# Performance work log

Hardware: AMD Instinct MI355X
Metric: run time of the kernel (lower is better)

## Reference

```python
import jax, jax.numpy as jnp
import numpy as np

DIM, K_NN, RADIUS, HIDDEN = 128, 4, 2.5, 64
B, T, N = 32, 64, 25


def setup_inputs() -> dict:
    key = jax.random.key(0)
    ks = jax.random.split(key, 12)
    s = 0.02
    return {
        "emb": jax.random.normal(ks[0], (B, T, N, DIM), jnp.float32),
        "bboxes": jax.random.uniform(ks[1], (B, T, N, 4), jnp.float32),
        "person_mask": jax.random.uniform(ks[2], (B, T, N)) < 0.9,
        "edge_w1": jax.random.normal(ks[3], (2 * DIM + 3, HIDDEN), jnp.float32) * s,
        "edge_b1": jnp.zeros((HIDDEN,), jnp.float32),
        "edge_w2": jax.random.normal(ks[4], (HIDDEN, DIM), jnp.float32) * s,
        "edge_b2": jnp.zeros((DIM,), jnp.float32),
        "node_w1": jax.random.normal(ks[5], (2 * DIM, HIDDEN), jnp.float32) * s,
        "node_b1": jnp.zeros((HIDDEN,), jnp.float32),
        "node_w2": jax.random.normal(ks[6], (HIDDEN, DIM), jnp.float32) * s,
        "node_b2": jnp.zeros((DIM,), jnp.float32),
        "ln_g": jnp.ones((DIM,), jnp.float32),
        "ln_b": jnp.zeros((DIM,), jnp.float32),
    }


def _forward(emb, bboxes, person_mask, edge_w1, edge_b1, edge_w2, edge_b2,
             node_w1, node_b1, node_w2, node_b2, ln_g, ln_b):
    b, t, n, d = emb.shape
    BT = b * t
    x = emb.reshape(BT, n, d)
    boxes = bboxes.reshape(BT, n, 4)
    mask = person_mask.reshape(BT, n)

    cx, cy = boxes[..., 0], boxes[..., 1]
    h = jnp.maximum(boxes[..., 3], 1e-6)
    dx = cx[:, :, None] - cx[:, None, :]            # [BT,N,N]
    dy = cy[:, :, None] - cy[:, None, :]
    dist = jnp.sqrt(dx * dx + dy * dy + 1e-6)
    scale = h[:, :, None]
    dx_n, dy_n, dist_n = dx / scale, dy / scale, dist / scale

    eye = jnp.eye(n, dtype=bool)[None]
    pair_valid = (mask[:, :, None] & mask[:, None, :]) & ~eye
    dist_for_knn = jnp.where(pair_valid, dist_n, 1e6)

    K = min(K_NN, max(n - 1, 1))
    neg_d, knn_idx = jax.lax.top_k(-dist_for_knn, K)  # smallest-K -> [BT,N,K]
    knn_dist = -neg_d

    nbr_valid = jnp.take_along_axis(pair_valid, knn_idx, axis=2)
    nbr_valid = nbr_valid & (knn_dist < RADIUS)

    # gather neighbor features: [BT,N,K,D]
    bt_idx = jnp.arange(BT)[:, None, None]
    x_j = x[bt_idx, knn_idx]
    x_i = jnp.broadcast_to(x[:, :, None, :], (BT, n, K, d))
    edge_all = jnp.stack([dx_n, dy_n, dist_n], axis=-1)  # [BT,N,N,3]
    e_ij = jnp.take_along_axis(edge_all, knn_idx[..., None], axis=2)  # [BT,N,K,3]

    msg_in = jnp.concatenate([x_i, x_j, e_ij], axis=-1)  # [BT,N,K,2D+3]
    msg = jax.nn.relu(msg_in @ edge_w1 + edge_b1) @ edge_w2 + edge_b2
    nbr_f = nbr_valid.astype(msg.dtype)
    msg = msg * nbr_f[..., None]
    denom = jnp.maximum(nbr_f.sum(axis=2, keepdims=True), 1.0)
    agg = msg.sum(axis=2) / denom                    # [BT,N,D]

    upd_in = jnp.concatenate([x, agg], axis=-1)
    delta = jax.nn.relu(upd_in @ node_w1 + node_b1) @ node_w2 + node_b2
    has_nbr = jnp.any(nbr_valid, axis=2, keepdims=True)
    delta = delta * has_nbr.astype(delta.dtype)

    y = x + delta
    mu = y.mean(axis=-1, keepdims=True)
    var = y.var(axis=-1, keepdims=True)
    y = (y - mu) * jax.lax.rsqrt(var + 1e-5) * ln_g + ln_b
    out = y * mask[..., None].astype(y.dtype)
    return out.reshape(b, t, n, d)


def reference(emb, bboxes, person_mask, edge_w1, edge_b1, edge_w2, edge_b2,
              node_w1, node_b1, node_w2, node_b2, ln_g, ln_b):
    return _forward(emb, bboxes, person_mask, edge_w1, edge_b1, edge_w2, edge_b2,
                    node_w1, node_b1, node_w2, node_b2, ln_g, ln_b)
```

## Files before the change

### kernel.cpp

```cpp
#include <hip/hip_runtime.h>

#define NN   25
#define DD   128
#define HH   64
#define KK   4
#define RADF 2.5f

#define XBP  136
#define HSP  72

#define O_W1T  0
#define O_W2NT 16896
#define O_N1LO 20992
#define O_N2T  29184
#define O_B2N  37376

typedef __attribute__((ext_vector_type(8))) short  short8;
typedef __attribute__((ext_vector_type(4))) float  f32x4;

__device__ __forceinline__ ushort f2bf(float x) {
    uint u = __float_as_uint(x);
    u += 0x7fffu + ((u >> 16) & 1u);
    return (ushort)(u >> 16);
}
__device__ __forceinline__ float bf2f(ushort u) {
    return __uint_as_float((uint)u << 16);
}
__device__ __forceinline__ uint pack2(float a, float b) {
    return (uint)f2bf(a) | ((uint)f2bf(b) << 16);
}
__device__ __forceinline__ short8 ldw(const ushort* p) {
    return *reinterpret_cast<const short8*>(p);
}
#define MFMA16(a, b, c) __builtin_amdgcn_mfma_f32_16x16x32_bf16((a), (b), (c), 0, 0, 0)

__global__ void prep_kernel(const float* __restrict__ ew1, const float* __restrict__ ew2,
                            const float* __restrict__ eb2, const float* __restrict__ nw1,
                            const float* __restrict__ nw2, ushort* __restrict__ w) {
    int tid = blockIdx.x * blockDim.x + threadIdx.x;
    int stride = gridDim.x * blockDim.x;
    for (int e = tid; e < 259 * 64; e += stride) {
        int k = e >> 6, c = e & 63;
        w[O_W1T + c * 264 + k] = f2bf(ew1[e]);
    }
    for (int e = tid; e < 64 * 128; e += stride) {
        int c = e >> 7, k = e & 127;
        w[O_N1LO + e] = f2bf(nw1[(size_t)k * 64 + c]);
    }
    for (int e = tid; e < 128 * 64; e += stride) {
        int d = e >> 6, k = e & 63;
        w[O_N2T + e] = f2bf(nw2[(size_t)k * 128 + d]);
    }
    for (int e = tid; e < 64 * 64; e += stride) {
        int c = e >> 6, k = e & 63;
        float acc = 0.f;
        for (int d = 0; d < DD; ++d)
            acc += ew2[(size_t)k * DD + d] * nw1[(size_t)(DD + d) * HH + c];
        w[O_W2NT + e] = f2bf(acc);
    }
    for (int c = tid; c < HH; c += stride) {
        float acc = 0.f;
        for (int d = 0; d < DD; ++d)
            acc += eb2[d] * nw1[(size_t)(DD + d) * HH + c];
        reinterpret_cast<float*>(w + O_B2N)[c] = acc;
    }
}

__global__ __launch_bounds__(128, 4) void ig12_kernel(
    const float* __restrict__ emb,
    const float* __restrict__ bboxes,
    const int*   __restrict__ pmask,
    const float* __restrict__ ew1f,
    const float* __restrict__ eb1,
    const float* __restrict__ nb1,
    const float* __restrict__ nb2,
    const float* __restrict__ lng,
    const float* __restrict__ lnb,
    const ushort* __restrict__ W,
    float* __restrict__ out)
{
    const int bt  = blockIdx.x;
    const int t   = threadIdx.x;
    const int wv  = t >> 6;
    const int ln  = t & 63;
    const int g   = ln >> 4;
    const int r16 = ln & 15;
    const int cb  = 2 * wv;
    const int cb4 = 4 * wv;

    __shared__ ushort s_xb[NN * XBP];
    __shared__ ushort s_hxi[NN * HSP];
    __shared__ ushort s_hs[NN * HSP];
    __shared__ ushort s_nxi[NN * HSP];
    __shared__ __align__(16) char s_misc[1600];
    __shared__ short  s_idxs[NN][KK];
    __shared__ float  s_meta[NN][4];

    float (*s_ev)[KK][4] = reinterpret_cast<float(*)[KK][4]>(s_misc);
    float (*s_red)[2][2] = reinterpret_cast<float(*)[2][2]>(s_misc);
    ushort* s_g1v = s_hxi;

    if (wv == 0) {
        const float4* src4 = reinterpret_cast<const float4*>(emb + (size_t)bt * (NN * DD));
        for (int u = ln; u < NN * 16; u += 64) {
            int row = u >> 4, q = u & 15;
            float4 f0 = src4[row * 32 + q * 2];
            float4 f1 = src4[row * 32 + q * 2 + 1];
            uint4 p;
            p.x = pack2(f0.x, f0.y); p.y = pack2(f0.z, f0.w);
            p.z = pack2(f1.x, f1.y); p.w = pack2(f1.z, f1.w);
            *reinterpret_cast<uint4*>(&s_xb[row * XBP + q * 8]) = p;
        }
    } else {
        const int n = (ln < NN) ? ln : NN - 1;
        const float4 b4 = *reinterpret_cast<const float4*>(bboxes + ((size_t)bt * NN + n) * 4);
        const float cxn = b4.x, cyn = b4.y;
        const float hvn = fmaxf(b4.w, 1e-6f);
        const int   mn  = pmask[(size_t)bt * NN + n];
        const float inv = 1.0f / hvn;
        float best[KK] = {1e30f, 1e30f, 1e30f, 1e30f};
        int   bidx[KK] = {0, 0, 0, 0};
        for (int j = 0; j < NN; ++j) {
            float cxj = __shfl(cxn, j);
            float cyj = __shfl(cyn, j);
            int   mj  = __shfl(mn, j);
            float dx = cxn - cxj, dy = cyn - cyj;
            float dn = sqrtf(fmaf(dx, dx, fmaf(dy, dy, 1e-6f))) * inv;
            bool  pv = (mn != 0) && (mj != 0) && (j != n);
            float cv = pv ? dn : 1e6f;
            int   ci = j;
#pragma unroll
            for (int kk = 0; kk < KK; ++kk) {
                if (cv < best[kk]) {
                    float tv = best[kk]; best[kk] = cv; cv = tv;
                    int   ti = bidx[kk]; bidx[kk] = ci; ci = ti;
                }
            }
        }
        float cnt = 0.f;
        float e0v[KK], e1v[KK], e2v[KK], vvv[KK];
#pragma unroll
        for (int k = 0; k < KK; ++k) {
            int bj = bidx[k];
            float cxb = __shfl(cxn, bj);
            float cyb = __shfl(cyn, bj);
            float val = (best[k] < RADF) ? 1.f : 0.f;
            cnt += val;
            float dx = cxn - cxb, dy = cyn - cyb;
            e0v[k] = dx * inv;
            e1v[k] = dy * inv;
            e2v[k] = sqrtf(fmaf(dx, dx, fmaf(dy, dy, 1e-6f))) * inv;
            vvv[k] = val;
        }
        if (ln < NN) {
#pragma unroll
            for (int k = 0; k < KK; ++k) {
                s_ev[n][k][0] = e0v[k];
                s_ev[n][k][1] = e1v[k];
                s_ev[n][k][2] = e2v[k];
                s_ev[n][k][3] = vvv[k];
                s_idxs[n][k]  = (short)bidx[k];
            }
            s_meta[n][0] = cnt;
            s_meta[n][1] = 1.0f / fmaxf(cnt, 1.0f);
            s_meta[n][2] = (cnt > 0.f) ? 1.f : 0.f;
            s_meta[n][3] = mn ? 1.f : 0.f;
        }
    }
    __syncthreads();

    {
        int na1 = 16 + r16; if (na1 > 24) na1 = 24;
        const ushort* A0 = s_xb + r16 * XBP + g * 8;
        const ushort* A1 = s_xb + na1 * XBP + g * 8;
        f32x4 ce[2][2] = {};
        f32x4 cn[2][2] = {};
#pragma unroll
        for (int kt = 0; kt < 4; ++kt) {
            short8 a0 = ldw(A0 + kt * 32);
            short8 a1 = ldw(A1 + kt * 32);
#pragma unroll
            for (int ntl = 0; ntl < 2; ++ntl) {
                short8 be = ldw(W + O_W1T  + (size_t)(16 * (cb + ntl) + r16) * 264 + kt * 32 + g * 8);
                short8 bn = ldw(W + O_N1LO + (size_t)(16 * (cb + ntl) + r16) * 128 + kt * 32 + g * 8);
                ce[0][ntl] = MFMA16(a0, be, ce[0][ntl]);
                ce[1][ntl] = MFMA16(a1, be, ce[1][ntl]);
                cn[0][ntl] = MFMA16(a0, bn, cn[0][ntl]);
                cn[1][ntl] = MFMA16(a1, bn, cn[1][ntl]);
            }
        }
#pragma unroll
        for (int mt = 0; mt < 2; ++mt)
#pragma unroll
            for (int q = 0; q < 4; ++q) {
                int nr = 16 * mt + 4 * g + q;
                if (nr < 25) {
#pragma unroll
                    for (int ntl = 0; ntl < 2; ++ntl) {
                        int col = 16 * (cb + ntl) + r16;
                        s_hxi[nr * HSP + col] = f2bf(ce[mt][ntl][q]);
                        s_nxi[nr * HSP + col] = f2bf(cn[mt][ntl][q]);
                    }
                }
            }
    }

    {
        int jn[7];
#pragma unroll
        for (int T = 0; T < 7; ++T) {
            int r = 16 * T + r16; if (r > 99) r = 99;
            jn[T] = s_idxs[r >> 2][r & 3];
        }
        f32x4 c[7][2] = {};
#pragma unroll
        for (int kt = 0; kt < 4; ++kt) {
            short8 b0 = ldw(W + O_W1T + (size_t)(16 * (cb + 0) + r16) * 264 + 128 + kt * 32 + g * 8);
            short8 b1 = ldw(W + O_W1T + (size_t)(16 * (cb + 1) + r16) * 264 + 128 + kt * 32 + g * 8);
#pragma unroll
            for (int T = 0; T < 7; ++T) {
                short8 a = ldw(s_xb + jn[T] * XBP + kt * 32 + g * 8);
                c[T][0] = MFMA16(a, b0, c[T][0]);
                c[T][1] = MFMA16(a, b1, c[T][1]);
            }
        }
        float we0[2], we1[2], we2[2], bb1[2];
#pragma unroll
        for (int ntl = 0; ntl < 2; ++ntl) {
            int col = 16 * (cb + ntl) + r16;
            we0[ntl] = ew1f[256 * 64 + col];
            we1[ntl] = ew1f[257 * 64 + col];
            we2[ntl] = ew1f[258 * 64 + col];
            bb1[ntl] = eb1[col];
        }
#pragma unroll
        for (int T = 0; T < 7; ++T) {
            const int n = 4 * T + g;
            if (n < 25) {
                float v0 = s_ev[n][0][3], v1 = s_ev[n][1][3];
                float v2 = s_ev[n][2][3], v3 = s_ev[n][3][3];
                float e0q[4], e1q[4], e2q[4];
#pragma unroll
                for (int q = 0; q < 4; ++q) {
                    e0q[q] = s_ev[n][q][0]; e1q[q] = s_ev[n][q][1]; e2q[q] = s_ev[n][q][2];
                }
#pragma unroll
                for (int ntl = 0; ntl < 2; ++ntl) {
                    int col = 16 * (cb + ntl) + r16;
                    float base = bb1[ntl] + bf2f(s_hxi[n * HSP + col]);
                    float p0 = c[T][ntl][0] + base + e0q[0] * we0[ntl] + e1q[0] * we1[ntl] + e2q[0] * we2[ntl];
                    float p1 = c[T][ntl][1] + base + e0q[1] * we0[ntl] + e1q[1] * we1[ntl] + e2q[1] * we2[ntl];
                    float p2 = c[T][ntl][2] + base + e0q[2] * we0[ntl] + e1q[2] * we1[ntl] + e2q[2] * we2[ntl];
                    float p3 = c[T][ntl][3] + base + e0q[3] * we0[ntl] + e1q[3] * we1[ntl] + e2q[3] * we2[ntl];
                    float hs = fmaf(v0, fmaxf(p0, 0.f),
                               fmaf(v1, fmaxf(p1, 0.f),
                               fmaf(v2, fmaxf(p2, 0.f),
                                    v3 * fmaxf(p3, 0.f))));
                    s_hs[n * HSP + col] = f2bf(hs);
                }
            }
        }
    }
    __syncthreads();

    {
        int na1 = 16 + r16; if (na1 > 24) na1 = 24;
        const ushort* A0 = s_hs + r16 * HSP + g * 8;
        const ushort* A1 = s_hs + na1 * HSP + g * 8;
        f32x4 c[2][2] = {};
#pragma unroll
        for (int kt = 0; kt < 2; ++kt) {
            short8 a0 = ldw(A0 + kt * 32);
            short8 a1 = ldw(A1 + kt * 32);
#pragma unroll
            for (int ntl = 0; ntl < 2; ++ntl) {
                short8 b = ldw(W + O_W2NT + (size_t)(16 * (cb + ntl) + r16) * 64 + kt * 32 + g * 8);
                c[0][ntl] = MFMA16(a0, b, c[0][ntl]);
                c[1][ntl] = MFMA16(a1, b, c[1][ntl]);
            }
        }
        const float* b2Np = reinterpret_cast<const float*>(W + O_B2N);
#pragma unroll
        for (int ntl = 0; ntl < 2; ++ntl) {
            int col = 16 * (cb + ntl) + r16;
            float b2n = b2Np[col];
            float b1c = nb1[col];
#pragma unroll
            for (int mt = 0; mt < 2; ++mt)
#pragma unroll
                for (int q = 0; q < 4; ++q) {
                    int nr = 16 * mt + 4 * g + q;
                    if (nr < 25) {
                        float v = bf2f(s_nxi[nr * HSP + col]) + b1c
                                + s_meta[nr][1] * fmaf(s_meta[nr][0], b2n, c[mt][ntl][q]);
                        s_g1v[nr * HSP + col] = f2bf(fmaxf(v, 0.f));
                    }
                }
        }
    }
    __syncthreads();

    {
        int na1 = 16 + r16; if (na1 > 24) na1 = 24;
        const ushort* A0 = s_g1v + r16 * HSP + g * 8;
        const ushort* A1 = s_g1v + na1 * HSP + g * 8;
        f32x4 c[2][4] = {};
#pragma unroll
        for (int kt = 0; kt < 2; ++kt) {
            short8 a0 = ldw(A0 + kt * 32);
            short8 a1 = ldw(A1 + kt * 32);
#pragma unroll
            for (int ntl = 0; ntl < 4; ++ntl) {
                short8 b = ldw(W + O_N2T + (size_t)(16 * (cb4 + ntl) + r16) * 64 + kt * 32 + g * 8);
                c[0][ntl] = MFMA16(a0, b, c[0][ntl]);
                c[1][ntl] = MFMA16(a1, b, c[1][ntl]);
            }
        }
        float nb2c[4], glc[4], blc[4];
#pragma unroll
        for (int ntl = 0; ntl < 4; ++ntl) {
            int col = 16 * (cb4 + ntl) + r16;
            nb2c[ntl] = nb2[col];
            glc[ntl]  = lng[col];
            blc[ntl]  = lnb[col];
        }
        float y[2][4][4];
#pragma unroll
        for (int mt = 0; mt < 2; ++mt) {
#pragma unroll
            for (int q = 0; q < 4; ++q) {
                int nr = 16 * mt + 4 * g + q;
                int nc = nr < 25 ? nr : 24;
                float has = s_meta[nc][2];
                float a = 0.f, b = 0.f;
#pragma unroll
                for (int ntl = 0; ntl < 4; ++ntl) {
                    int col = 16 * (cb4 + ntl) + r16;
                    float yv = fmaf(has, c[mt][ntl][q] + nb2c[ntl], bf2f(s_xb[nc * XBP + col]));
                    y[mt][ntl][q] = yv;
                    a += yv;
                    b = fmaf(yv, yv, b);
                }
#pragma unroll
                for (int o = 1; o < 16; o <<= 1) {
                    a += __shfl_xor(a, o);
                    b += __shfl_xor(b, o);
                }
                if (r16 == 0 && nr < 25) {
                    s_red[nr][wv][0] = a;
                    s_red[nr][wv][1] = b;
                }
            }
        }
        __syncthreads();
#pragma unroll
        for (int mt = 0; mt < 2; ++mt) {
#pragma unroll
            for (int q = 0; q < 4; ++q) {
                int nr = 16 * mt + 4 * g + q;
                int nc = nr < 25 ? nr : 24;
                float S   = s_red[nc][0][0] + s_red[nc][1][0];
                float S2  = s_red[nc][0][1] + s_red[nc][1][1];
                float mu  = S * (1.0f / 128.0f);
                float var = S2 * (1.0f / 128.0f) - mu * mu;
                float rs  = rsqrtf(var + 1e-5f);
                float mk  = s_meta[nc][3];
                if (nr < 25) {
                    float* op = out + (size_t)bt * (NN * DD) + nr * DD;
#pragma unroll
                    for (int ntl = 0; ntl < 4; ++ntl) {
                        int col = 16 * (cb4 + ntl) + r16;
                        op[col] = fmaf((y[mt][ntl][q] - mu) * rs, glc[ntl], blc[ntl]) * mk;
                    }
                }
            }
        }
    }
}

extern "C" void kernel_launch(void* const* d_in, const int* in_sizes, int n_in,
                              void* d_out, int out_size, void* d_ws, size_t ws_size,
                              hipStream_t stream) {
    const float* emb    = (const float*)d_in[0];
    const float* bboxes = (const float*)d_in[1];
    const int*   pmask  = (const int*)  d_in[2];
    const float* ew1    = (const float*)d_in[3];
    const float* eb1    = (const float*)d_in[4];
    const float* ew2    = (const float*)d_in[5];
    const float* eb2    = (const float*)d_in[6];
    const float* nw1    = (const float*)d_in[7];
    const float* nb1    = (const float*)d_in[8];
    const float* nw2    = (const float*)d_in[9];
    const float* nb2    = (const float*)d_in[10];
    const float* lng    = (const float*)d_in[11];
    const float* lnb    = (const float*)d_in[12];
    float* out = (float*)d_out;
    ushort* W  = (ushort*)d_ws;

    prep_kernel<<<64, 256, 0, stream>>>(ew1, ew2, eb2, nw1, nw2, W);

    const int BT = in_sizes[2] / NN;
    ig12_kernel<<<BT, 128, 0, stream>>>(
        emb, bboxes, pmask, ew1, eb1, nb1, nb2, lng, lnb, W, out);
}
```

Before: 42.73 us.

## Keep node pre-activation in registers, prefetch weights across barriers, use LDS-only barriers

The node-MLP x-part accumulator stays in registers instead of round-tripping through a shared buffer, which removes that LDS array and its stores and loads. Global weight and bias loads for the next two GEMM stages are issued before each barrier so their latency overlaps the barrier wait. __syncthreads is replaced by an explicit lgkmcnt(0) wait plus s_barrier, so the barrier does not wait on outstanding global loads. The cost is higher register pressure from live accumulators and prefetched fragments, which could reduce occupancy or cause spills.

```diff
diff --git a/kernel.cpp b/kernel.cpp
--- a/kernel.cpp
+++ b/kernel.cpp
@@ -33,6 +33,11 @@
     return *reinterpret_cast<const short8*>(p);
 }
 #define MFMA16(a, b, c) __builtin_amdgcn_mfma_f32_16x16x32_bf16((a), (b), (c), 0, 0, 0)
+
+#define BAR_LGKM() do {                                      \
+    asm volatile("s_waitcnt lgkmcnt(0)" ::: "memory");       \
+    __builtin_amdgcn_s_barrier();                            \
+} while (0)
 
 __global__ void prep_kernel(const float* __restrict__ ew1, const float* __restrict__ ew2,
                             const float* __restrict__ eb2, const float* __restrict__ nw1,
@@ -66,7 +71,7 @@
     }
 }
 
-__global__ __launch_bounds__(128, 4) void ig12_kernel(
+__global__ __launch_bounds__(128, 4) void ig13_kernel(
     const float* __restrict__ emb,
     const float* __restrict__ bboxes,
     const int*   __restrict__ pmask,
@@ -91,7 +96,6 @@
     __shared__ ushort s_xb[NN * XBP];
     __shared__ ushort s_hxi[NN * HSP];
     __shared__ ushort s_hs[NN * HSP];
-    __shared__ ushort s_nxi[NN * HSP];
     __shared__ __align__(16) char s_misc[1600];
     __shared__ short  s_idxs[NN][KK];
     __shared__ float  s_meta[NN][4];
@@ -167,14 +171,14 @@
             s_meta[n][3] = mn ? 1.f : 0.f;
         }
     }
-    __syncthreads();
-
+    BAR_LGKM();
+
+    f32x4 cn[2][2] = {};
     {
         int na1 = 16 + r16; if (na1 > 24) na1 = 24;
         const ushort* A0 = s_xb + r16 * XBP + g * 8;
         const ushort* A1 = s_xb + na1 * XBP + g * 8;
         f32x4 ce[2][2] = {};
-        f32x4 cn[2][2] = {};
 #pragma unroll
         for (int kt = 0; kt < 4; ++kt) {
             short8 a0 = ldw(A0 + kt * 32);
@@ -199,7 +203,6 @@
                     for (int ntl = 0; ntl < 2; ++ntl) {
                         int col = 16 * (cb + ntl) + r16;
                         s_hxi[nr * HSP + col] = f2bf(ce[mt][ntl][q]);
-                        s_nxi[nr * HSP + col] = f2bf(cn[mt][ntl][q]);
                     }
                 }
             }
@@ -261,7 +264,24 @@
             }
         }
     }
-    __syncthreads();
+
+    short8 pfN1[2][2];
+    float  pf_b2n[2], pf_b1c[2];
+    {
+        const float* b2Np = reinterpret_cast<const float*>(W + O_B2N);
+#pragma unroll
+        for (int kt = 0; kt < 2; ++kt)
+#pragma unroll
+            for (int ntl = 0; ntl < 2; ++ntl)
+                pfN1[kt][ntl] = ldw(W + O_W2NT + (size_t)(16 * (cb + ntl) + r16) * 64 + kt * 32 + g * 8);
+#pragma unroll
+        for (int ntl = 0; ntl < 2; ++ntl) {
+            int col = 16 * (cb + ntl) + r16;
+            pf_b2n[ntl] = b2Np[col];
+            pf_b1c[ntl] = nb1[col];
+        }
+    }
+    BAR_LGKM();
 
     {
         int na1 = 16 + r16; if (na1 > 24) na1 = 24;
@@ -274,55 +294,59 @@
             short8 a1 = ldw(A1 + kt * 32);
 #pragma unroll
             for (int ntl = 0; ntl < 2; ++ntl) {
-                short8 b = ldw(W + O_W2NT + (size_t)(16 * (cb + ntl) + r16) * 64 + kt * 32 + g * 8);
-                c[0][ntl] = MFMA16(a0, b, c[0][ntl]);
-                c[1][ntl] = MFMA16(a1, b, c[1][ntl]);
-            }
-        }
-        const float* b2Np = reinterpret_cast<const float*>(W + O_B2N);
+                c[0][ntl] = MFMA16(a0, pfN1[kt][ntl], c[0][ntl]);
+                c[1][ntl] = MFMA16(a1, pfN1[kt][ntl], c[1][ntl]);
+            }
+        }
 #pragma unroll
         for (int ntl = 0; ntl < 2; ++ntl) {
-            int col = 16 * (cb + ntl) + r16;
-            float b2n = b2Np[col];
-            float b1c = nb1[col];
 #pragma unroll
             for (int mt = 0; mt < 2; ++mt)
 #pragma unroll
                 for (int q = 0; q < 4; ++q) {
                     int nr = 16 * mt + 4 * g + q;
                     if (nr < 25) {
-                        float v = bf2f(s_nxi[nr * HSP + col]) + b1c
-                                + s_meta[nr][1] * fmaf(s_meta[nr][0], b2n, c[mt][ntl][q]);
+                        int col = 16 * (cb + ntl) + r16;
+                        float v = cn[mt][ntl][q] + pf_b1c[ntl]
+                                + s_meta[nr][1] * fmaf(s_meta[nr][0], pf_b2n[ntl], c[mt][ntl][q]);
                         s_g1v[nr * HSP + col] = f2bf(fmaxf(v, 0.f));
                     }
                 }
         }
     }
-    __syncthreads();
-
-    {
-        int na1 = 16 + r16; if (na1 > 24) na1 = 24;
-        const ushort* A0 = s_g1v + r16 * HSP + g * 8;
-        const ushort* A1 = s_g1v + na1 * HSP + g * 8;
-        f32x4 c[2][4] = {};
-#pragma unroll
-        for (int kt = 0; kt < 2; ++kt) {
-            short8 a0 = ldw(A0 + kt * 32);
-            short8 a1 = ldw(A1 + kt * 32);
-#pragma unroll
-            for (int ntl = 0; ntl < 4; ++ntl) {
-                short8 b = ldw(W + O_N2T + (size_t)(16 * (cb4 + ntl) + r16) * 64 + kt * 32 + g * 8);
-                c[0][ntl] = MFMA16(a0, b, c[0][ntl]);
-                c[1][ntl] = MFMA16(a1, b, c[1][ntl]);
-            }
-        }
-        float nb2c[4], glc[4], blc[4];
+
+    short8 pfN2[2][4];
+    float  nb2c[4], glc[4], blc[4];
+    {
+#pragma unroll
+        for (int kt = 0; kt < 2; ++kt)
+#pragma unroll
+            for (int ntl = 0; ntl < 4; ++ntl)
+                pfN2[kt][ntl] = ldw(W + O_N2T + (size_t)(16 * (cb4 + ntl) + r16) * 64 + kt * 32 + g * 8);
 #pragma unroll
         for (int ntl = 0; ntl < 4; ++ntl) {
             int col = 16 * (cb4 + ntl) + r16;
             nb2c[ntl] = nb2[col];
             glc[ntl]  = lng[col];
             blc[ntl]  = lnb[col];
+        }
+    }
+    BAR_LGKM();
+
+    {
+        int na1 = 16 + r16; if (na1 > 24) na1 = 24;
+        const ushort* A0 = s_g1v + r16 * HSP + g * 8;
+        const ushort* A1 = s_g1v + na1 * HSP + g * 8;
+        f32x4 c[2][4] = {};
+#pragma unroll
+        for (int kt = 0; kt < 2; ++kt) {
+            short8 a0 = ldw(A0 + kt * 32);
+            short8 a1 = ldw(A1 + kt * 32);
+#pragma unroll
+            for (int ntl = 0; ntl < 4; ++ntl) {
+                c[0][ntl] = MFMA16(a0, pfN2[kt][ntl], c[0][ntl]);
+                c[1][ntl] = MFMA16(a1, pfN2[kt][ntl], c[1][ntl]);
+            }
         }
         float y[2][4][4];
 #pragma unroll
@@ -352,7 +376,7 @@
                 }
             }
         }
-        __syncthreads();
+        BAR_LGKM();
 #pragma unroll
         for (int mt = 0; mt < 2; ++mt) {
 #pragma unroll
@@ -400,6 +424,6 @@
     prep_kernel<<<64, 256, 0, stream>>>(ew1, ew2, eb2, nw1, nw2, W);
 
     const int BT = in_sizes[2] / NN;
-    ig12_kernel<<<BT, 128, 0, stream>>>(
+    ig13_kernel<<<BT, 128, 0, stream>>>(
         emb, bboxes, pmask, ew1, eb1, nb1, nb2, lng, lnb, W, out);
 }
```

Measured after the change: 51.72 us. 1.21x slower.

## Fuse edge-MLP first layer into one per-edge MFMA over x_i, x_j and edge features

Applied to the files above, without the earlier changes.

The edge first-layer GEMM now runs directly on per-edge rows [x_i | x_j | e_ij, 1], with the bias folded into an extended padded weight matrix (288 columns). This removes the separate x_i projection, its bf16 staging in shared memory, and the scalar FMA epilogue for edge features. It also keeps the node-update x projection in registers instead of shared memory, merges the scratch buffers to cut LDS use, and raises launch bounds to 5 blocks. The trade-off is redundant x_i MFMA work, since x_i is recomputed per edge instead of per node, plus bf16 rounding of the edge features.

```diff
diff --git a/kernel.cpp b/kernel.cpp
--- a/kernel.cpp
+++ b/kernel.cpp
@@ -9,11 +9,11 @@
 #define XBP  136
 #define HSP  72
 
-#define O_W1T  0
-#define O_W2NT 16896
-#define O_N1LO 20992
-#define O_N2T  29184
-#define O_B2N  37376
+#define O_W1U  0
+#define O_W2NT 18432
+#define O_N1LO 22528
+#define O_N2T  30720
+#define O_B2N  38912
 
 typedef __attribute__((ext_vector_type(8))) short  short8;
 typedef __attribute__((ext_vector_type(4))) float  f32x4;
@@ -34,14 +34,16 @@
 }
 #define MFMA16(a, b, c) __builtin_amdgcn_mfma_f32_16x16x32_bf16((a), (b), (c), 0, 0, 0)
 
-__global__ void prep_kernel(const float* __restrict__ ew1, const float* __restrict__ ew2,
-                            const float* __restrict__ eb2, const float* __restrict__ nw1,
-                            const float* __restrict__ nw2, ushort* __restrict__ w) {
+__global__ void prep_kernel(const float* __restrict__ ew1, const float* __restrict__ eb1,
+                            const float* __restrict__ ew2, const float* __restrict__ eb2,
+                            const float* __restrict__ nw1, const float* __restrict__ nw2,
+                            ushort* __restrict__ w) {
     int tid = blockIdx.x * blockDim.x + threadIdx.x;
     int stride = gridDim.x * blockDim.x;
-    for (int e = tid; e < 259 * 64; e += stride) {
-        int k = e >> 6, c = e & 63;
-        w[O_W1T + c * 264 + k] = f2bf(ew1[e]);
+    for (int e = tid; e < 64 * 288; e += stride) {
+        int c = e / 288, k = e % 288;
+        float v = (k < 259) ? ew1[(size_t)k * 64 + c] : (k == 259 ? eb1[c] : 0.f);
+        w[O_W1U + e] = f2bf(v);
     }
     for (int e = tid; e < 64 * 128; e += stride) {
         int c = e >> 7, k = e & 127;
@@ -66,12 +68,10 @@
     }
 }
 
-__global__ __launch_bounds__(128, 4) void ig12_kernel(
+__global__ __launch_bounds__(128, 5) void ig14_kernel(
     const float* __restrict__ emb,
     const float* __restrict__ bboxes,
     const int*   __restrict__ pmask,
-    const float* __restrict__ ew1f,
-    const float* __restrict__ eb1,
     const float* __restrict__ nb1,
     const float* __restrict__ nb2,
     const float* __restrict__ lng,
@@ -85,20 +85,19 @@
     const int ln  = t & 63;
     const int g   = ln >> 4;
     const int r16 = ln & 15;
+    const int rq  = r16 >> 2;
+    const int ke3 = r16 & 3;
     const int cb  = 2 * wv;
     const int cb4 = 4 * wv;
 
     __shared__ ushort s_xb[NN * XBP];
-    __shared__ ushort s_hxi[NN * HSP];
-    __shared__ ushort s_hs[NN * HSP];
-    __shared__ ushort s_nxi[NN * HSP];
-    __shared__ __align__(16) char s_misc[1600];
+    __shared__ ushort s_h[NN * HSP];
+    __shared__ __align__(16) ushort s_epk[NN][KK][8];
+    __shared__ float  s_val[NN][KK];
     __shared__ short  s_idxs[NN][KK];
     __shared__ float  s_meta[NN][4];
 
-    float (*s_ev)[KK][4] = reinterpret_cast<float(*)[KK][4]>(s_misc);
-    float (*s_red)[2][2] = reinterpret_cast<float(*)[2][2]>(s_misc);
-    ushort* s_g1v = s_hxi;
+    float (*s_red)[2][2] = reinterpret_cast<float(*)[2][2]>(&s_epk[0][0][0]);
 
     if (wv == 0) {
         const float4* src4 = reinterpret_cast<const float4*>(emb + (size_t)bt * (NN * DD));
@@ -155,11 +154,14 @@
         if (ln < NN) {
 #pragma unroll
             for (int k = 0; k < KK; ++k) {
-                s_ev[n][k][0] = e0v[k];
-                s_ev[n][k][1] = e1v[k];
-                s_ev[n][k][2] = e2v[k];
-                s_ev[n][k][3] = vvv[k];
-                s_idxs[n][k]  = (short)bidx[k];
+                s_epk[n][k][0] = f2bf(e0v[k]);
+                s_epk[n][k][1] = f2bf(e1v[k]);
+                s_epk[n][k][2] = f2bf(e2v[k]);
+                s_epk[n][k][3] = 0x3F80;
+                s_epk[n][k][4] = 0; s_epk[n][k][5] = 0;
+                s_epk[n][k][6] = 0; s_epk[n][k][7] = 0;
+                s_val[n][k]  = vvv[k];
+                s_idxs[n][k] = (short)bidx[k];
             }
             s_meta[n][0] = cnt;
             s_meta[n][1] = 1.0f / fmaxf(cnt, 1.0f);
@@ -169,104 +171,84 @@
     }
     __syncthreads();
 
+#pragma unroll
+    for (int pass = 0; pass < 2; ++pass) {
+        const int t0 = pass ? 4 : 0;
+        const int nT = pass ? 3 : 4;
+        int na_[4], jn[4];
+#pragma unroll
+        for (int i = 0; i < 4; ++i) {
+            if (i < nT) {
+                int v = 4 * (t0 + i) + rq; if (v > 24) v = 24;
+                na_[i] = v;
+                jn[i]  = s_idxs[v][ke3];
+            } else { na_[i] = 24; jn[i] = 0; }
+        }
+        f32x4 c[4][2] = {};
+#pragma unroll
+        for (int kt = 0; kt < 9; ++kt) {
+            short8 b0 = ldw(W + O_W1U + (size_t)(16 * (cb + 0) + r16) * 288 + kt * 32 + g * 8);
+            short8 b1 = ldw(W + O_W1U + (size_t)(16 * (cb + 1) + r16) * 288 + kt * 32 + g * 8);
+#pragma unroll
+            for (int i = 0; i < 4; ++i) {
+                if (i < nT) {
+                    short8 a;
+                    if (kt < 4)      a = ldw(s_xb + na_[i] * XBP + kt * 32 + g * 8);
+                    else if (kt < 8) a = ldw(s_xb + jn[i] * XBP + (kt - 4) * 32 + g * 8);
+                    else {
+                        short8 z = {0, 0, 0, 0, 0, 0, 0, 0};
+                        a = z;
+                        if (g == 0) a = ldw(&s_epk[na_[i]][ke3][0]);
+                    }
+                    c[i][0] = MFMA16(a, b0, c[i][0]);
+                    c[i][1] = MFMA16(a, b1, c[i][1]);
+                }
+            }
+        }
+#pragma unroll
+        for (int i = 0; i < 4; ++i) {
+            if (i < nT) {
+                const int n = 4 * (t0 + i) + g;
+                if (n < 25) {
+                    float v0 = s_val[n][0], v1 = s_val[n][1];
+                    float v2 = s_val[n][2], v3 = s_val[n][3];
+#pragma unroll
+                    for (int ntl = 0; ntl < 2; ++ntl) {
+                        int col = 16 * (cb + ntl) + r16;
+                        float hs = fmaf(v0, fmaxf(c[i][ntl][0], 0.f),
+                                   fmaf(v1, fmaxf(c[i][ntl][1], 0.f),
+                                   fmaf(v2, fmaxf(c[i][ntl][2], 0.f),
+                                        v3 * fmaxf(c[i][ntl][3], 0.f))));
+                        s_h[n * HSP + col] = f2bf(hs);
+                    }
+                }
+            }
+        }
+    }
+
+    f32x4 cn[2][2] = {};
     {
         int na1 = 16 + r16; if (na1 > 24) na1 = 24;
         const ushort* A0 = s_xb + r16 * XBP + g * 8;
         const ushort* A1 = s_xb + na1 * XBP + g * 8;
-        f32x4 ce[2][2] = {};
-        f32x4 cn[2][2] = {};
 #pragma unroll
         for (int kt = 0; kt < 4; ++kt) {
             short8 a0 = ldw(A0 + kt * 32);
             short8 a1 = ldw(A1 + kt * 32);
 #pragma unroll
             for (int ntl = 0; ntl < 2; ++ntl) {
-                short8 be = ldw(W + O_W1T  + (size_t)(16 * (cb + ntl) + r16) * 264 + kt * 32 + g * 8);
                 short8 bn = ldw(W + O_N1LO + (size_t)(16 * (cb + ntl) + r16) * 128 + kt * 32 + g * 8);
-                ce[0][ntl] = MFMA16(a0, be, ce[0][ntl]);
-                ce[1][ntl] = MFMA16(a1, be, ce[1][ntl]);
                 cn[0][ntl] = MFMA16(a0, bn, cn[0][ntl]);
                 cn[1][ntl] = MFMA16(a1, bn, cn[1][ntl]);
             }
         }
-#pragma unroll
-        for (int mt = 0; mt < 2; ++mt)
-#pragma unroll
-            for (int q = 0; q < 4; ++q) {
-                int nr = 16 * mt + 4 * g + q;
-                if (nr < 25) {
-#pragma unroll
-                    for (int ntl = 0; ntl < 2; ++ntl) {
-                        int col = 16 * (cb + ntl) + r16;
-                        s_hxi[nr * HSP + col] = f2bf(ce[mt][ntl][q]);
-                        s_nxi[nr * HSP + col] = f2bf(cn[mt][ntl][q]);
-                    }
-                }
-            }
-    }
-
-    {
-        int jn[7];
-#pragma unroll
-        for (int T = 0; T < 7; ++T) {
-            int r = 16 * T + r16; if (r > 99) r = 99;
-            jn[T] = s_idxs[r >> 2][r & 3];
-        }
-        f32x4 c[7][2] = {};
-#pragma unroll
-        for (int kt = 0; kt < 4; ++kt) {
-            short8 b0 = ldw(W + O_W1T + (size_t)(16 * (cb + 0) + r16) * 264 + 128 + kt * 32 + g * 8);
-            short8 b1 = ldw(W + O_W1T + (size_t)(16 * (cb + 1) + r16) * 264 + 128 + kt * 32 + g * 8);
-#pragma unroll
-            for (int T = 0; T < 7; ++T) {
-                short8 a = ldw(s_xb + jn[T] * XBP + kt * 32 + g * 8);
-                c[T][0] = MFMA16(a, b0, c[T][0]);
-                c[T][1] = MFMA16(a, b1, c[T][1]);
-            }
-        }
-        float we0[2], we1[2], we2[2], bb1[2];
-#pragma unroll
-        for (int ntl = 0; ntl < 2; ++ntl) {
-            int col = 16 * (cb + ntl) + r16;
-            we0[ntl] = ew1f[256 * 64 + col];
-            we1[ntl] = ew1f[257 * 64 + col];
-            we2[ntl] = ew1f[258 * 64 + col];
-            bb1[ntl] = eb1[col];
-        }
-#pragma unroll
-        for (int T = 0; T < 7; ++T) {
-            const int n = 4 * T + g;
-            if (n < 25) {
-                float v0 = s_ev[n][0][3], v1 = s_ev[n][1][3];
-                float v2 = s_ev[n][2][3], v3 = s_ev[n][3][3];
-                float e0q[4], e1q[4], e2q[4];
-#pragma unroll
-                for (int q = 0; q < 4; ++q) {
-                    e0q[q] = s_ev[n][q][0]; e1q[q] = s_ev[n][q][1]; e2q[q] = s_ev[n][q][2];
-                }
-#pragma unroll
-                for (int ntl = 0; ntl < 2; ++ntl) {
-                    int col = 16 * (cb + ntl) + r16;
-                    float base = bb1[ntl] + bf2f(s_hxi[n * HSP + col]);
-                    float p0 = c[T][ntl][0] + base + e0q[0] * we0[ntl] + e1q[0] * we1[ntl] + e2q[0] * we2[ntl];
-                    float p1 = c[T][ntl][1] + base + e0q[1] * we0[ntl] + e1q[1] * we1[ntl] + e2q[1] * we2[ntl];
-                    float p2 = c[T][ntl][2] + base + e0q[2] * we0[ntl] + e1q[2] * we1[ntl] + e2q[2] * we2[ntl];
-                    float p3 = c[T][ntl][3] + base + e0q[3] * we0[ntl] + e1q[3] * we1[ntl] + e2q[3] * we2[ntl];
-                    float hs = fmaf(v0, fmaxf(p0, 0.f),
-                               fmaf(v1, fmaxf(p1, 0.f),
-                               fmaf(v2, fmaxf(p2, 0.f),
-                                    v3 * fmaxf(p3, 0.f))));
-                    s_hs[n * HSP + col] = f2bf(hs);
-                }
-            }
-        }
     }
     __syncthreads();
 
     {
         int na1 = 16 + r16; if (na1 > 24) na1 = 24;
-        const ushort* A0 = s_hs + r16 * HSP + g * 8;
-        const ushort* A1 = s_hs + na1 * HSP + g * 8;
+        const ushort* A0 = s_h + r16 * HSP + g * 8;
+        const ushort* A1 = s_h + na1 * HSP + g * 8;
         f32x4 c[2][2] = {};
 #pragma unroll
         for (int kt = 0; kt < 2; ++kt) {
@@ -279,6 +261,7 @@
                 c[1][ntl] = MFMA16(a1, b, c[1][ntl]);
             }
         }
+        __syncthreads();
         const float* b2Np = reinterpret_cast<const float*>(W + O_B2N);
 #pragma unroll
         for (int ntl = 0; ntl < 2; ++ntl) {
@@ -291,9 +274,9 @@
                 for (int q = 0; q < 4; ++q) {
                     int nr = 16 * mt + 4 * g + q;
                     if (nr < 25) {
-                        float v = bf2f(s_nxi[nr * HSP + col]) + b1c
+                        float v = cn[mt][ntl][q] + b1c
                                 + s_meta[nr][1] * fmaf(s_meta[nr][0], b2n, c[mt][ntl][q]);
-                        s_g1v[nr * HSP + col] = f2bf(fmaxf(v, 0.f));
+                        s_h[nr * HSP + col] = f2bf(fmaxf(v, 0.f));
                     }
                 }
         }
@@ -302,8 +285,8 @@
 
     {
         int na1 = 16 + r16; if (na1 > 24) na1 = 24;
-        const ushort* A0 = s_g1v + r16 * HSP + g * 8;
-        const ushort* A1 = s_g1v + na1 * HSP + g * 8;
+        const ushort* A0 = s_h + r16 * HSP + g * 8;
+        const ushort* A1 = s_h + na1 * HSP + g * 8;
         f32x4 c[2][4] = {};
 #pragma unroll
         for (int kt = 0; kt < 2; ++kt) {
@@ -397,9 +380,9 @@
     float* out = (float*)d_out;
     ushort* W  = (ushort*)d_ws;
 
-    prep_kernel<<<64, 256, 0, stream>>>(ew1, ew2, eb2, nw1, nw2, W);
+    prep_kernel<<<64, 256, 0, stream>>>(ew1, eb1, ew2, eb2, nw1, nw2, W);
 
     const int BT = in_sizes[2] / NN;
-    ig12_kernel<<<BT, 128, 0, stream>>>(
-        emb, bboxes, pmask, ew1, eb1, nb1, nb2, lng, lnb, W, out);
-}
+    ig14_kernel<<<BT, 128, 0, stream>>>(
+        emb, bboxes, pmask, nb1, nb2, lng, lnb, W, out);
+}
```

New measurement: 49.17 us. 15.1% more time.

## Split each frame's 25 nodes across two blocks to double grid parallelism

Applied to the files above, without the earlier changes.

Each block now handles 13 or 12 of a frame's 25 nodes, and the grid is launched with twice as many blocks. The node-wise MFMA tiles shrink from two 16-row tiles to one, and the shared buffers are sized for 13 nodes. Occupancy bounds are raised from 4 to 6 blocks per SM. In exchange, every block still loads the full frame embedding, repeats the kNN computation for all nodes, and re-reads the weights, so that redundant work doubles.

```diff
diff --git a/kernel.cpp b/kernel.cpp
--- a/kernel.cpp
+++ b/kernel.cpp
@@ -5,6 +5,7 @@
 #define HH   64
 #define KK   4
 #define RADF 2.5f
+#define NMX  13
 
 #define XBP  136
 #define HSP  72
@@ -66,7 +67,7 @@
     }
 }
 
-__global__ __launch_bounds__(128, 4) void ig12_kernel(
+__global__ __launch_bounds__(128, 6) void ig15_kernel(
     const float* __restrict__ emb,
     const float* __restrict__ bboxes,
     const int*   __restrict__ pmask,
@@ -79,7 +80,13 @@
     const ushort* __restrict__ W,
     float* __restrict__ out)
 {
-    const int bt  = blockIdx.x;
+    const int blk  = blockIdx.x;
+    const int bt   = blk >> 1;
+    const int half = blk & 1;
+    const int NB   = half ? 13 : 0;
+    const int NM   = half ? 12 : 13;
+    const int nT   = half ? 3 : 4;
+
     const int t   = threadIdx.x;
     const int wv  = t >> 6;
     const int ln  = t & 63;
@@ -89,15 +96,14 @@
     const int cb4 = 4 * wv;
 
     __shared__ ushort s_xb[NN * XBP];
-    __shared__ ushort s_hxi[NN * HSP];
-    __shared__ ushort s_hs[NN * HSP];
-    __shared__ ushort s_nxi[NN * HSP];
-    __shared__ __align__(16) char s_misc[1600];
-    __shared__ short  s_idxs[NN][KK];
-    __shared__ float  s_meta[NN][4];
-
-    float (*s_ev)[KK][4] = reinterpret_cast<float(*)[KK][4]>(s_misc);
-    float (*s_red)[2][2] = reinterpret_cast<float(*)[2][2]>(s_misc);
+    __shared__ ushort s_hxi[NMX * HSP];
+    __shared__ ushort s_hs[NMX * HSP];
+    __shared__ ushort s_nxi[NMX * HSP];
+    __shared__ float  s_ev[NMX][KK][4];
+    __shared__ short  s_idxs[NMX][KK];
+    __shared__ float  s_meta[NMX][4];
+
+    float (*s_red)[2][2] = reinterpret_cast<float(*)[2][2]>(&s_ev[0][0][0]);
     ushort* s_g1v = s_hxi;
 
     if (wv == 0) {
@@ -152,76 +158,76 @@
             e2v[k] = sqrtf(fmaf(dx, dx, fmaf(dy, dy, 1e-6f))) * inv;
             vvv[k] = val;
         }
-        if (ln < NN) {
+        if (ln >= NB && ln < NB + NM) {
+            const int nl = ln - NB;
 #pragma unroll
             for (int k = 0; k < KK; ++k) {
-                s_ev[n][k][0] = e0v[k];
-                s_ev[n][k][1] = e1v[k];
-                s_ev[n][k][2] = e2v[k];
-                s_ev[n][k][3] = vvv[k];
-                s_idxs[n][k]  = (short)bidx[k];
-            }
-            s_meta[n][0] = cnt;
-            s_meta[n][1] = 1.0f / fmaxf(cnt, 1.0f);
-            s_meta[n][2] = (cnt > 0.f) ? 1.f : 0.f;
-            s_meta[n][3] = mn ? 1.f : 0.f;
+                s_ev[nl][k][0] = e0v[k];
+                s_ev[nl][k][1] = e1v[k];
+                s_ev[nl][k][2] = e2v[k];
+                s_ev[nl][k][3] = vvv[k];
+                s_idxs[nl][k]  = (short)bidx[k];
+            }
+            s_meta[nl][0] = cnt;
+            s_meta[nl][1] = 1.0f / fmaxf(cnt, 1.0f);
+            s_meta[nl][2] = (cnt > 0.f) ? 1.f : 0.f;
+            s_meta[nl][3] = mn ? 1.f : 0.f;
         }
     }
     __syncthreads();
 
     {
-        int na1 = 16 + r16; if (na1 > 24) na1 = 24;
-        const ushort* A0 = s_xb + r16 * XBP + g * 8;
-        const ushort* A1 = s_xb + na1 * XBP + g * 8;
-        f32x4 ce[2][2] = {};
-        f32x4 cn[2][2] = {};
+        const int rl = (r16 < NM) ? r16 : NM - 1;
+        const ushort* A0 = s_xb + (NB + rl) * XBP + g * 8;
+        f32x4 ce[2] = {};
+        f32x4 cn_[2] = {};
 #pragma unroll
         for (int kt = 0; kt < 4; ++kt) {
             short8 a0 = ldw(A0 + kt * 32);
-            short8 a1 = ldw(A1 + kt * 32);
 #pragma unroll
             for (int ntl = 0; ntl < 2; ++ntl) {
                 short8 be = ldw(W + O_W1T  + (size_t)(16 * (cb + ntl) + r16) * 264 + kt * 32 + g * 8);
                 short8 bn = ldw(W + O_N1LO + (size_t)(16 * (cb + ntl) + r16) * 128 + kt * 32 + g * 8);
-                ce[0][ntl] = MFMA16(a0, be, ce[0][ntl]);
-                ce[1][ntl] = MFMA16(a1, be, ce[1][ntl]);
-                cn[0][ntl] = MFMA16(a0, bn, cn[0][ntl]);
-                cn[1][ntl] = MFMA16(a1, bn, cn[1][ntl]);
-            }
-        }
-#pragma unroll
-        for (int mt = 0; mt < 2; ++mt)
-#pragma unroll
-            for (int q = 0; q < 4; ++q) {
-                int nr = 16 * mt + 4 * g + q;
-                if (nr < 25) {
-#pragma unroll
-                    for (int ntl = 0; ntl < 2; ++ntl) {
-                        int col = 16 * (cb + ntl) + r16;
-                        s_hxi[nr * HSP + col] = f2bf(ce[mt][ntl][q]);
-                        s_nxi[nr * HSP + col] = f2bf(cn[mt][ntl][q]);
-                    }
-                }
-            }
+                ce[ntl]  = MFMA16(a0, be, ce[ntl]);
+                cn_[ntl] = MFMA16(a0, bn, cn_[ntl]);
+            }
+        }
+#pragma unroll
+        for (int q = 0; q < 4; ++q) {
+            int nr = 4 * g + q;
+            if (nr < NM) {
+#pragma unroll
+                for (int ntl = 0; ntl < 2; ++ntl) {
+                    int col = 16 * (cb + ntl) + r16;
+                    s_hxi[nr * HSP + col] = f2bf(ce[ntl][q]);
+                    s_nxi[nr * HSP + col] = f2bf(cn_[ntl][q]);
+                }
+            }
+        }
     }
 
     {
-        int jn[7];
-#pragma unroll
-        for (int T = 0; T < 7; ++T) {
-            int r = 16 * T + r16; if (r > 99) r = 99;
-            jn[T] = s_idxs[r >> 2][r & 3];
-        }
-        f32x4 c[7][2] = {};
+        const int ME = NM * KK;
+        int jn[4];
+#pragma unroll
+        for (int T = 0; T < 4; ++T) {
+            if (T < nT) {
+                int lr = 16 * T + r16; if (lr > ME - 1) lr = ME - 1;
+                jn[T] = s_idxs[lr >> 2][lr & 3];
+            } else jn[T] = 0;
+        }
+        f32x4 c[4][2] = {};
 #pragma unroll
         for (int kt = 0; kt < 4; ++kt) {
             short8 b0 = ldw(W + O_W1T + (size_t)(16 * (cb + 0) + r16) * 264 + 128 + kt * 32 + g * 8);
             short8 b1 = ldw(W + O_W1T + (size_t)(16 * (cb + 1) + r16) * 264 + 128 + kt * 32 + g * 8);
 #pragma unroll
-            for (int T = 0; T < 7; ++T) {
-                short8 a = ldw(s_xb + jn[T] * XBP + kt * 32 + g * 8);
-                c[T][0] = MFMA16(a, b0, c[T][0]);
-                c[T][1] = MFMA16(a, b1, c[T][1]);
+            for (int T = 0; T < 4; ++T) {
+                if (T < nT) {
+                    short8 a = ldw(s_xb + jn[T] * XBP + kt * 32 + g * 8);
+                    c[T][0] = MFMA16(a, b0, c[T][0]);
+                    c[T][1] = MFMA16(a, b1, c[T][1]);
+                }
             }
         }
         float we0[2], we1[2], we2[2], bb1[2];
@@ -234,29 +240,31 @@
             bb1[ntl] = eb1[col];
         }
 #pragma unroll
-        for (int T = 0; T < 7; ++T) {
-            const int n = 4 * T + g;
-            if (n < 25) {
-                float v0 = s_ev[n][0][3], v1 = s_ev[n][1][3];
-                float v2 = s_ev[n][2][3], v3 = s_ev[n][3][3];
-                float e0q[4], e1q[4], e2q[4];
-#pragma unroll
-                for (int q = 0; q < 4; ++q) {
-                    e0q[q] = s_ev[n][q][0]; e1q[q] = s_ev[n][q][1]; e2q[q] = s_ev[n][q][2];
-                }
-#pragma unroll
-                for (int ntl = 0; ntl < 2; ++ntl) {
-                    int col = 16 * (cb + ntl) + r16;
-                    float base = bb1[ntl] + bf2f(s_hxi[n * HSP + col]);
-                    float p0 = c[T][ntl][0] + base + e0q[0] * we0[ntl] + e1q[0] * we1[ntl] + e2q[0] * we2[ntl];
-                    float p1 = c[T][ntl][1] + base + e0q[1] * we0[ntl] + e1q[1] * we1[ntl] + e2q[1] * we2[ntl];
-                    float p2 = c[T][ntl][2] + base + e0q[2] * we0[ntl] + e1q[2] * we1[ntl] + e2q[2] * we2[ntl];
-                    float p3 = c[T][ntl][3] + base + e0q[3] * we0[ntl] + e1q[3] * we1[ntl] + e2q[3] * we2[ntl];
-                    float hs = fmaf(v0, fmaxf(p0, 0.f),
-                               fmaf(v1, fmaxf(p1, 0.f),
-                               fmaf(v2, fmaxf(p2, 0.f),
-                                    v3 * fmaxf(p3, 0.f))));
-                    s_hs[n * HSP + col] = f2bf(hs);
+        for (int T = 0; T < 4; ++T) {
+            if (T < nT) {
+                const int n = 4 * T + g;
+                if (n < NM) {
+                    float v0 = s_ev[n][0][3], v1 = s_ev[n][1][3];
+                    float v2 = s_ev[n][2][3], v3 = s_ev[n][3][3];
+                    float e0q[4], e1q[4], e2q[4];
+#pragma unroll
+                    for (int q = 0; q < 4; ++q) {
+                        e0q[q] = s_ev[n][q][0]; e1q[q] = s_ev[n][q][1]; e2q[q] = s_ev[n][q][2];
+                    }
+#pragma unroll
+                    for (int ntl = 0; ntl < 2; ++ntl) {
+                        int col = 16 * (cb + ntl) + r16;
+                        float base = bb1[ntl] + bf2f(s_hxi[n * HSP + col]);
+                        float p0 = c[T][ntl][0] + base + e0q[0] * we0[ntl] + e1q[0] * we1[ntl] + e2q[0] * we2[ntl];
+                        float p1 = c[T][ntl][1] + base + e0q[1] * we0[ntl] + e1q[1] * we1[ntl] + e2q[1] * we2[ntl];
+                        float p2 = c[T][ntl][2] + base + e0q[2] * we0[ntl] + e1q[2] * we1[ntl] + e2q[2] * we2[ntl];
+                        float p3 = c[T][ntl][3] + base + e0q[3] * we0[ntl] + e1q[3] * we1[ntl] + e2q[3] * we2[ntl];
+                        float hs = fmaf(v0, fmaxf(p0, 0.f),
+                                   fmaf(v1, fmaxf(p1, 0.f),
+                                   fmaf(v2, fmaxf(p2, 0.f),
+                                        v3 * fmaxf(p3, 0.f))));
+                        s_hs[n * HSP + col] = f2bf(hs);
+                    }
                 }
             }
         }
@@ -264,19 +272,16 @@
     __syncthreads();
 
     {
-        int na1 = 16 + r16; if (na1 > 24) na1 = 24;
-        const ushort* A0 = s_hs + r16 * HSP + g * 8;
-        const ushort* A1 = s_hs + na1 * HSP + g * 8;
-        f32x4 c[2][2] = {};
+        const int rl = (r16 < NM) ? r16 : NM - 1;
+        const ushort* A0 = s_hs + rl * HSP + g * 8;
+        f32x4 c[2] = {};
 #pragma unroll
         for (int kt = 0; kt < 2; ++kt) {
             short8 a0 = ldw(A0 + kt * 32);
-            short8 a1 = ldw(A1 + kt * 32);
 #pragma unroll
             for (int ntl = 0; ntl < 2; ++ntl) {
                 short8 b = ldw(W + O_W2NT + (size_t)(16 * (cb + ntl) + r16) * 64 + kt * 32 + g * 8);
-                c[0][ntl] = MFMA16(a0, b, c[0][ntl]);
-                c[1][ntl] = MFMA16(a1, b, c[1][ntl]);
+                c[ntl] = MFMA16(a0, b, c[ntl]);
             }
         }
         const float* b2Np = reinterpret_cast<const float*>(W + O_B2N);
@@ -286,34 +291,29 @@
             float b2n = b2Np[col];
             float b1c = nb1[col];
 #pragma unroll
-            for (int mt = 0; mt < 2; ++mt)
-#pragma unroll
-                for (int q = 0; q < 4; ++q) {
-                    int nr = 16 * mt + 4 * g + q;
-                    if (nr < 25) {
-                        float v = bf2f(s_nxi[nr * HSP + col]) + b1c
-                                + s_meta[nr][1] * fmaf(s_meta[nr][0], b2n, c[mt][ntl][q]);
-                        s_g1v[nr * HSP + col] = f2bf(fmaxf(v, 0.f));
-                    }
-                }
+            for (int q = 0; q < 4; ++q) {
+                int nr = 4 * g + q;
+                if (nr < NM) {
+                    float v = bf2f(s_nxi[nr * HSP + col]) + b1c
+                            + s_meta[nr][1] * fmaf(s_meta[nr][0], b2n, c[ntl][q]);
+                    s_g1v[nr * HSP + col] = f2bf(fmaxf(v, 0.f));
+                }
+            }
         }
     }
     __syncthreads();
 
     {
-        int na1 = 16 + r16; if (na1 > 24) na1 = 24;
-        const ushort* A0 = s_g1v + r16 * HSP + g * 8;
-        const ushort* A1 = s_g1v + na1 * HSP + g * 8;
-        f32x4 c[2][4] = {};
+        const int rl = (r16 < NM) ? r16 : NM - 1;
+        const ushort* A0 = s_g1v + rl * HSP + g * 8;
+        f32x4 c[4] = {};
 #pragma unroll
         for (int kt = 0; kt < 2; ++kt) {
             short8 a0 = ldw(A0 + kt * 32);
-            short8 a1 = ldw(A1 + kt * 32);
 #pragma unroll
             for (int ntl = 0; ntl < 4; ++ntl) {
                 short8 b = ldw(W + O_N2T + (size_t)(16 * (cb4 + ntl) + r16) * 64 + kt * 32 + g * 8);
-                c[0][ntl] = MFMA16(a0, b, c[0][ntl]);
-                c[1][ntl] = MFMA16(a1, b, c[1][ntl]);
+                c[ntl] = MFMA16(a0, b, c[ntl]);
             }
         }
         float nb2c[4], glc[4], blc[4];
@@ -324,54 +324,48 @@
             glc[ntl]  = lng[col];
             blc[ntl]  = lnb[col];
         }
-        float y[2][4][4];
-#pragma unroll
-        for (int mt = 0; mt < 2; ++mt) {
-#pragma unroll
-            for (int q = 0; q < 4; ++q) {
-                int nr = 16 * mt + 4 * g + q;
-                int nc = nr < 25 ? nr : 24;
-                float has = s_meta[nc][2];
-                float a = 0.f, b = 0.f;
+        float y[4][4];
+#pragma unroll
+        for (int q = 0; q < 4; ++q) {
+            int nr = 4 * g + q;
+            int nc = nr < NM ? nr : NM - 1;
+            float has = s_meta[nc][2];
+            float a = 0.f, b = 0.f;
+#pragma unroll
+            for (int ntl = 0; ntl < 4; ++ntl) {
+                int col = 16 * (cb4 + ntl) + r16;
+                float yv = fmaf(has, c[ntl][q] + nb2c[ntl], bf2f(s_xb[(NB + nc) * XBP + col]));
+                y[ntl][q] = yv;
+                a += yv;
+                b = fmaf(yv, yv, b);
+            }
+#pragma unroll
+            for (int o = 1; o < 16; o <<= 1) {
+                a += __shfl_xor(a, o);
+                b += __shfl_xor(b, o);
+            }
+            if (r16 == 0 && nr < NM) {
+                s_red[nr][wv][0] = a;
+                s_red[nr][wv][1] = b;
+            }
+        }
+        __syncthreads();
+#pragma unroll
+        for (int q = 0; q < 4; ++q) {
+            int nr = 4 * g + q;
+            int nc = nr < NM ? nr : NM - 1;
+            float S   = s_red[nc][0][0] + s_red[nc][1][0];
+            float S2  = s_red[nc][0][1] + s_red[nc][1][1];
+            float mu  = S * (1.0f / 128.0f);
+            float var = S2 * (1.0f / 128.0f) - mu * mu;
+            float rs  = rsqrtf(var + 1e-5f);
+            float mk  = s_meta[nc][3];
+            if (nr < NM) {
+                float* op = out + ((size_t)bt * NN + NB + nr) * DD;
 #pragma unroll
                 for (int ntl = 0; ntl < 4; ++ntl) {
                     int col = 16 * (cb4 + ntl) + r16;
-                    float yv = fmaf(has, c[mt][ntl][q] + nb2c[ntl], bf2f(s_xb[nc * XBP + col]));
-                    y[mt][ntl][q] = yv;
-                    a += yv;
-                    b = fmaf(yv, yv, b);
-                }
-#pragma unroll
-                for (int o = 1; o < 16; o <<= 1) {
-                    a += __shfl_xor(a, o);
-                    b += __shfl_xor(b, o);
-                }
-                if (r16 == 0 && nr < 25) {
-                    s_red[nr][wv][0] = a;
-                    s_red[nr][wv][1] = b;
-                }
-            }
-        }
-        __syncthreads();
-#pragma unroll
-        for (int mt = 0; mt < 2; ++mt) {
-#pragma unroll
-            for (int q = 0; q < 4; ++q) {
-                int nr = 16 * mt + 4 * g + q;
-                int nc = nr < 25 ? nr : 24;
-                float S   = s_red[nc][0][0] + s_red[nc][1][0];
-                float S2  = s_red[nc][0][1] + s_red[nc][1][1];
-                float mu  = S * (1.0f / 128.0f);
-                float var = S2 * (1.0f / 128.0f) - mu * mu;
-                float rs  = rsqrtf(var + 1e-5f);
-                float mk  = s_meta[nc][3];
-                if (nr < 25) {
-                    float* op = out + (size_t)bt * (NN * DD) + nr * DD;
-#pragma unroll
-                    for (int ntl = 0; ntl < 4; ++ntl) {
-                        int col = 16 * (cb4 + ntl) + r16;
-                        op[col] = fmaf((y[mt][ntl][q] - mu) * rs, glc[ntl], blc[ntl]) * mk;
-                    }
+                    op[col] = fmaf((y[ntl][q] - mu) * rs, glc[ntl], blc[ntl]) * mk;
                 }
             }
         }
@@ -400,6 +394,6 @@
     prep_kernel<<<64, 256, 0, stream>>>(ew1, ew2, eb2, nw1, nw2, W);
 
     const int BT = in_sizes[2] / NN;
-    ig12_kernel<<<BT, 128, 0, stream>>>(
+    ig15_kernel<<<BT * 2, 128, 0, stream>>>(
         emb, bboxes, pmask, ew1, eb1, nb1, nb2, lng, lnb, W, out);
 }
```

Result: slower. 56.68 us (+32.6%).
